# Performance work log

Measured on AMD Instinct MI355X. Metric: run time of the kernel, lower is better.

The kernel has to match this reference:

```python
import jax, jax.numpy as jnp
import numpy as np

DIM = 128
HEADS = 32
DIM_HEAD = 64
INNER = DIM * DIM_HEAD  # 8192, as written in the source (dim * dim_head)
D = INNER // HEADS      # 256 per-head dim
B, N = 1, 2048
ROT = 64                # partial rotary width (l)
SCALE = DIM ** (-0.5)   # source uses dim**-0.5, not head-dim


def _rotate_half(x):
    # x: [..., l]; split as (j d) with j=2 -> cat(-x2, x1)
    x1, x2 = jnp.split(x, 2, axis=-1)
    return jnp.concatenate((-x2, x1), axis=-1)


def _apply_rotary(q, k, freqs):
    # freqs: [n, l]; q,k: [b,h,n,d] with l <= d (partial rotary)
    l = freqs.shape[-1]
    cos, sin = jnp.cos(freqs), jnp.sin(freqs)  # broadcast over b,h
    ql, qr = q[..., :l], q[..., l:]
    kl, kr = k[..., :l], k[..., l:]
    ql = ql * cos + _rotate_half(ql) * sin
    kl = kl * cos + _rotate_half(kl) * sin
    return jnp.concatenate((ql, qr), axis=-1), jnp.concatenate((kl, kr), axis=-1)


def setup_inputs() -> dict:
    key = jax.random.key(0)
    k1, k2, k3, k4, k5 = jax.random.split(key, 5)
    return {
        "x": jax.random.normal(k1, (B, N, DIM), dtype=jnp.float32),
        "Wqkv": jax.random.normal(k2, (3 * INNER, DIM), dtype=jnp.float32) * 0.02,
        "Wproj": jax.random.normal(k3, (DIM, INNER), dtype=jnp.float32) * 0.02,
        "bproj": jax.random.normal(k4, (DIM,), dtype=jnp.float32) * 0.02,
        "rotary_pos_emb": jax.random.normal(k5, (N, ROT), dtype=jnp.float32),
    }


def reference(x, Wqkv, Wproj, bproj, rotary_pos_emb):
    b, n, _ = x.shape
    qkv = x @ Wqkv.T                                   # [b, n, 3*inner]
    qkv = qkv.reshape(b, n, 3, HEADS, D)               # (qkv h d) ordering
    qkv = jnp.transpose(qkv, (2, 0, 3, 1, 4))          # [3, b, h, n, d]
    q, k, v = qkv[0], qkv[1], qkv[2]
    q, k = _apply_rotary(q, k, rotary_pos_emb)
    energy = jnp.einsum("bhid,bhjd->bhij", q, k) * SCALE  # [b,h,n,n]
    attn = jax.nn.softmax(energy, axis=-1)
    out = jnp.einsum("bhij,bhjd->bhid", attn, v)       # [b,h,n,d]
    out = jnp.transpose(out, (0, 2, 1, 3)).reshape(b, n, INNER)
    return out @ Wproj.T + bproj
```

## Files before the change

### kernel.cpp

```cpp
#include <hip/hip_runtime.h>


typedef unsigned short u16;
typedef unsigned int u32;
typedef __attribute__((ext_vector_type(8))) u16 u16x8;
typedef __attribute__((ext_vector_type(8))) __bf16 bf16x8;
typedef __attribute__((ext_vector_type(4))) float f32x4;
typedef __attribute__((ext_vector_type(16))) float f32x16;
typedef __attribute__((ext_vector_type(4))) u32 u32x4;
typedef __attribute__((ext_vector_type(2))) u32 u32x2;

#define DEV static __device__ __forceinline__

DEV u16 f2b(float f) {
  __bf16 h = (__bf16)f;
  return __builtin_bit_cast(u16, h);
}
DEV float b2f(u16 b) {
  u32 u = ((u32)b) << 16;
  return __builtin_bit_cast(float, u);
}
DEV u32 pk2(float a, float b) { return (u32)f2b(a) | ((u32)f2b(b) << 16); }

DEV f32x4 mfma16(u16x8 a, u16x8 b, f32x4 c) {
  return __builtin_amdgcn_mfma_f32_16x16x32_bf16(
      __builtin_bit_cast(bf16x8, a), __builtin_bit_cast(bf16x8, b), c, 0, 0, 0);
}
DEV f32x16 mfma32(u16x8 a, u16x8 b, f32x16 c) {
  return __builtin_amdgcn_mfma_f32_32x32x16_bf16(
      __builtin_bit_cast(bf16x8, a), __builtin_bit_cast(bf16x8, b), c, 0, 0, 0);
}

DEV int swz(int row, int kelem, int rowBytes) {
  return row * rowBytes + ((kelem * 2) ^ ((row & 7) << 4));
}

DEV void dma16(const void* g, void* l) {
  __builtin_amdgcn_global_load_lds(
      (const __attribute__((address_space(1))) void*)g,
      (__attribute__((address_space(3))) void*)l, 16, 0, 0);
}

__global__ __launch_bounds__(256) void k_cvt(const float* __restrict__ src,
                                             u16* __restrict__ dst, int n8) {
  int i = blockIdx.x * 256 + threadIdx.x;
  if (i >= n8) return;
  const float4* s = (const float4*)src;
  float4 a = s[i * 2], b = s[i * 2 + 1];
  u16x8 o;
  o[0] = f2b(a.x); o[1] = f2b(a.y); o[2] = f2b(a.z); o[3] = f2b(a.w);
  o[4] = f2b(b.x); o[5] = f2b(b.y); o[6] = f2b(b.z); o[7] = f2b(b.w);
  *(u16x8*)(dst + (size_t)i * 8) = o;
}

__global__ __launch_bounds__(256) void k_qkv(const u16* __restrict__ xb,
                                             const u16* __restrict__ wb,
                                             u16* __restrict__ qw,
                                             u16* __restrict__ kw,
                                             u16* __restrict__ vw) {
  __shared__ char lds[65536];
  const int tid = threadIdx.x;
  const int rt = blockIdx.x % 192, nt = blockIdx.x / 192;
  const int r0 = rt * 128, n0 = nt * 128;
#pragma unroll
  for (int p = 0; p < 8; ++p) {
    int row = p * 16 + (tid >> 4);
    int k0 = (tid & 15) * 8;
    *(u16x8*)(lds + swz(row, k0, 256)) =
        *(const u16x8*)(wb + (size_t)(r0 + row) * 128 + k0);
    *(u16x8*)(lds + 32768 + swz(row, k0, 256)) =
        *(const u16x8*)(xb + (size_t)(n0 + row) * 128 + k0);
  }
  __syncthreads();
  const int wid = tid >> 6, lane = tid & 63, lq = lane & 15, g = lane >> 4;
  const int wr = wid >> 1, wn = wid & 1;
  const bool isV = (r0 >= 16384);
  f32x4 acc[4][4] = {};
#pragma unroll
  for (int ks = 0; ks < 4; ++ks) {
    u16x8 wa[4], xa[4];
#pragma unroll
    for (int i = 0; i < 4; ++i) {
      int rw = wr * 64 + i * 16 + lq;
      wa[i] = *(const u16x8*)(lds + swz(rw, ks * 32 + g * 8, 256));
      int rx = wn * 64 + i * 16 + lq;
      xa[i] = *(const u16x8*)(lds + 32768 + swz(rx, ks * 32 + g * 8, 256));
    }
    if (!isV) {
#pragma unroll
      for (int i = 0; i < 4; ++i)
#pragma unroll
        for (int j = 0; j < 4; ++j) acc[i][j] = mfma16(wa[i], xa[j], acc[i][j]);
    } else {
#pragma unroll
      for (int i = 0; i < 4; ++i)
#pragma unroll
        for (int j = 0; j < 4; ++j) acc[i][j] = mfma16(xa[j], wa[i], acc[i][j]);
    }
  }
  const float SMQ = 0.08838834764831845f * 1.4426950408889634f;
  if (!isV) {
#pragma unroll
    for (int i = 0; i < 4; ++i) {
      int rb = r0 + wr * 64 + i * 16 + g * 4;
      u16* dst0 = (rb >= 8192) ? kw : qw;
      float scl = (rb >= 8192) ? 1.0f : SMQ;
      int hd = rb & 8191;
      int h = hd >> 8, db = hd & 255;
#pragma unroll
      for (int j = 0; j < 4; ++j) {
        int n = n0 + wn * 64 + j * 16 + lq;
        u32x2 pk;
        pk.x = pk2(acc[i][j][0] * scl, acc[i][j][1] * scl);
        pk.y = pk2(acc[i][j][2] * scl, acc[i][j][3] * scl);
        *(u32x2*)(dst0 + ((size_t)h * 2048 + n) * 256 + db) = pk;
      }
    }
  } else {
#pragma unroll
    for (int i = 0; i < 4; ++i) {
      int rc = r0 - 16384 + wr * 64 + i * 16 + lq;
      int h = rc >> 8, d = rc & 255;
#pragma unroll
      for (int j = 0; j < 4; ++j) {
        int nb = n0 + wn * 64 + j * 16 + g * 4;
        u32x2 pk;
        pk.x = pk2(acc[i][j][0], acc[i][j][1]);
        pk.y = pk2(acc[i][j][2], acc[i][j][3]);
        *(u32x2*)(vw + ((size_t)h * 256 + d) * 2048 + nb) = pk;
      }
    }
  }
}

__global__ __launch_bounds__(256) void k_rope(u16* __restrict__ qw,
                                              u16* __restrict__ kw,
                                              const float* __restrict__ fr) {
  int idx = blockIdx.x * 256 + threadIdx.x;
  int seg = idx & 3;
  int n = (idx >> 2) & 2047;
  int h = (idx >> 13) & 31;
  u16* base = ((idx >> 18) ? kw : qw) + ((size_t)h * 2048 + n) * 256 + seg * 8;
  u16x8 lo = *(const u16x8*)base;
  u16x8 hi = *(const u16x8*)(base + 32);
  const float* f = fr + n * 64 + seg * 8;
  u16x8 nlo, nhi;
#pragma unroll
  for (int e = 0; e < 8; ++e) {
    float fl = f[e], fh = f[e + 32];
    float sl, cl, sh, ch;
    __sincosf(fl, &sl, &cl);
    __sincosf(fh, &sh, &ch);
    float a = b2f(lo[e]), b = b2f(hi[e]);
    nlo[e] = f2b(a * cl - b * sl);
    nhi[e] = f2b(b * ch + a * sh);
  }
  *(u16x8*)base = nlo;
  *(u16x8*)(base + 32) = nhi;
}

__global__ __launch_bounds__(512, 2) void k_attn(const u16* __restrict__ qw,
                                                 const u16* __restrict__ kw,
                                                 const u16* __restrict__ vw,
                                                 u16* __restrict__ ow) {
  __shared__ char lds[98304];
  const int tid = threadIdx.x;
  const int h = blockIdx.x & 31;
  const int qb = blockIdx.x >> 5;
  const int wid = tid >> 6, lane = tid & 63;
  const int l31 = lane & 31, h2 = lane >> 5;
  const int q0w = qb * 256 + wid * 32;
  const int lane16 = lane * 16;

  const u16* kbase = kw + (size_t)h * 2048 * 256;
  const u16* vbase = vw + (size_t)h * 256 * 2048;

  const bool isK = (wid < 4);
  const int dstslot = isK ? wid * 4 : 16 + (wid - 4) * 4;
  int off[4];
#pragma unroll
  for (int i = 0; i < 4; ++i) {
    if (isK) {
      int s = wid * 4 + i;
      off[i] = l31 * 256 + s * 16 + h2 * 8;
    } else {
      int u = (wid - 4) * 4 + i;
      off[i] = ((u >> 1) * 32 + l31) * 2048 + (u & 1) * 16 + h2 * 8;
    }
  }

  u16x8 qf[16];
  {
    const u16* qp = qw + ((size_t)h * 2048 + q0w + l31) * 256 + h2 * 8;
#pragma unroll
    for (int dt = 0; dt < 16; ++dt) qf[dt] = *(const u16x8*)(qp + dt * 16);
  }

  f32x16 oacc[8] = {};
  float mrun = -1e30f, lrun = 0.f;

#define STAGE(T, BUF)                                               \
  {                                                                 \
    const int kv0_ = (T) * 32;                                      \
    char* b_ = lds + (BUF) * 32768;                                 \
    if (isK) {                                                      \
      _Pragma("unroll") for (int i = 0; i < 4; ++i)                 \
          dma16(kbase + (size_t)kv0_ * 256 + off[i],                \
                b_ + (dstslot + i) * 1024);                         \
    } else {                                                        \
      _Pragma("unroll") for (int i = 0; i < 4; ++i)                 \
          dma16(vbase + kv0_ + off[i], b_ + (dstslot + i) * 1024);  \
    }                                                               \
  }

  STAGE(0, 0);
  STAGE(1, 1);
  int rb = 0, sb = 2;

  for (int t = 0; t < 64; ++t) {
    if (t < 63)
      asm volatile("s_waitcnt vmcnt(4)" ::: "memory");
    else
      asm volatile("s_waitcnt vmcnt(0)" ::: "memory");
    __builtin_amdgcn_s_barrier();
    asm volatile("" ::: "memory");
    if (t < 62) STAGE(t + 2, sb);

    const char* kb = lds + rb * 32768;

    f32x16 sa = {};
    __builtin_amdgcn_s_setprio(1);
#pragma unroll
    for (int dt = 0; dt < 16; ++dt) {
      u16x8 ka = *(const u16x8*)(kb + dt * 1024 + lane16);
      sa = mfma32(ka, qf[dt], sa);
    }
    __builtin_amdgcn_s_setprio(0);

    float m8[8];
#pragma unroll
    for (int r = 0; r < 8; ++r) m8[r] = fmaxf(sa[r], sa[r + 8]);
#pragma unroll
    for (int r = 0; r < 4; ++r) m8[r] = fmaxf(m8[r], m8[r + 4]);
    float mt = fmaxf(fmaxf(m8[0], m8[1]), fmaxf(m8[2], m8[3]));
    mt = fmaxf(mt, __shfl_xor(mt, 32));
    if (!__all(mt - mrun <= 8.0f)) {
      float mnew = fmaxf(mrun, mt);
      float corr = __builtin_amdgcn_exp2f(mrun - mnew);
      lrun *= corr;
#pragma unroll
      for (int dt = 0; dt < 8; ++dt)
#pragma unroll
        for (int r = 0; r < 16; ++r) oacc[dt][r] *= corr;
      mrun = mnew;
    }
    float p[16];
#pragma unroll
    for (int r = 0; r < 16; ++r)
      p[r] = __builtin_amdgcn_exp2f(sa[r] - mrun);
    float s8[8];
#pragma unroll
    for (int r = 0; r < 8; ++r) s8[r] = p[r] + p[r + 8];
#pragma unroll
    for (int r = 0; r < 4; ++r) s8[r] = s8[r] + s8[r + 4];
    float lt = (s8[0] + s8[1]) + (s8[2] + s8[3]);
    lt += __shfl_xor(lt, 32);
    lrun += lt;

    u32 pkk[8], xpk[8];
#pragma unroll
    for (int j = 0; j < 8; ++j) pkk[j] = pk2(p[2 * j], p[2 * j + 1]);
#pragma unroll
    for (int j = 0; j < 8; ++j) xpk[j] = (u32)__shfl_xor((int)pkk[j], 32);
    u32x4 b0v, b1v;
    b0v[0] = h2 ? xpk[2] : pkk[0];
    b0v[1] = h2 ? xpk[3] : pkk[1];
    b0v[2] = h2 ? pkk[2] : xpk[0];
    b0v[3] = h2 ? pkk[3] : xpk[1];
    b1v[0] = h2 ? xpk[6] : pkk[4];
    b1v[1] = h2 ? xpk[7] : pkk[5];
    b1v[2] = h2 ? pkk[6] : xpk[4];
    b1v[3] = h2 ? pkk[7] : xpk[5];
    u16x8 pb0 = __builtin_bit_cast(u16x8, b0v);
    u16x8 pb1 = __builtin_bit_cast(u16x8, b1v);

    __builtin_amdgcn_s_setprio(1);
#pragma unroll
    for (int dt = 0; dt < 8; ++dt) {
      u16x8 v0 = *(const u16x8*)(kb + 16384 + (dt * 2) * 1024 + lane16);
      oacc[dt] = mfma32(v0, pb0, oacc[dt]);
      u16x8 v1 = *(const u16x8*)(kb + 16384 + (dt * 2 + 1) * 1024 + lane16);
      oacc[dt] = mfma32(v1, pb1, oacc[dt]);
    }
    __builtin_amdgcn_s_setprio(0);

    rb = (rb == 2) ? 0 : rb + 1;
    sb = (sb == 2) ? 0 : sb + 1;
  }
#undef STAGE

  float inv = 1.0f / lrun;
  u16* orow = ow + (size_t)(q0w + l31) * 8192 + h * 256 + h2 * 4;
#pragma unroll
  for (int dt = 0; dt < 8; ++dt)
#pragma unroll
    for (int k = 0; k < 4; ++k) {
      u32x2 o2;
      o2.x = pk2(oacc[dt][4 * k] * inv, oacc[dt][4 * k + 1] * inv);
      o2.y = pk2(oacc[dt][4 * k + 2] * inv, oacc[dt][4 * k + 3] * inv);
      *(u32x2*)(orow + dt * 32 + k * 8) = o2;
    }
}

__global__ __launch_bounds__(256) void k_proj(const u16* __restrict__ ow,
                                              const u16* __restrict__ wp,
                                              float* __restrict__ part) {
  __shared__ char lds[49152];
  const int tid = threadIdx.x;
  const int nt = blockIdx.x >> 3, kc = blockIdx.x & 7;
  const int n0 = nt * 64, kb = kc * 1024;
  const int wid = tid >> 6, lane = tid & 63, lq = lane & 15, g = lane >> 4;
  f32x4 acc[8] = {};
  for (int kt = 0; kt < 8; ++kt) {
    int kk = kb + kt * 128;
#pragma unroll
    for (int p = 0; p < 4; ++p) {
      int nr = p * 16 + (tid >> 4);
      int k0 = (tid & 15) * 8;
      *(u16x8*)(lds + swz(nr, k0, 256)) =
          *(const u16x8*)(ow + (size_t)(n0 + nr) * 8192 + kk + k0);
    }
#pragma unroll
    for (int p = 0; p < 8; ++p) {
      int er = p * 16 + (tid >> 4);
      int k0 = (tid & 15) * 8;
      *(u16x8*)(lds + 16384 + swz(er, k0, 256)) =
          *(const u16x8*)(wp + (size_t)er * 8192 + kk + k0);
    }
    __syncthreads();
#pragma unroll
    for (int ks = 0; ks < 4; ++ks) {
      int nr = wid * 16 + lq;
      u16x8 oa = *(const u16x8*)(lds + swz(nr, ks * 32 + g * 8, 256));
#pragma unroll
      for (int ef = 0; ef < 8; ++ef) {
        int er = ef * 16 + lq;
        u16x8 wf = *(const u16x8*)(lds + 16384 + swz(er, ks * 32 + g * 8, 256));
        acc[ef] = mfma16(oa, wf, acc[ef]);
      }
    }
    __syncthreads();
  }
  float* pb = part + (size_t)kc * 262144;
#pragma unroll
  for (int ef = 0; ef < 8; ++ef)
#pragma unroll
    for (int r = 0; r < 4; ++r) {
      int n = n0 + wid * 16 + g * 4 + r;
      pb[n * 128 + ef * 16 + lq] = acc[ef][r];
    }
}

__global__ __launch_bounds__(256) void k_reduce(const float* __restrict__ part,
                                                const float* __restrict__ bias,
                                                float* __restrict__ out) {
  int i = blockIdx.x * 256 + threadIdx.x;
  float s = bias[i & 127];
#pragma unroll
  for (int c = 0; c < 8; ++c) s += part[(size_t)c * 262144 + i];
  out[i] = s;
}

extern "C" void kernel_launch(void* const* d_in, const int* in_sizes, int n_in,
                              void* d_out, int out_size, void* d_ws, size_t ws_size,
                              hipStream_t stream) {
  const float* x = (const float*)d_in[0];
  const float* wqkv = (const float*)d_in[1];
  const float* wproj = (const float*)d_in[2];
  const float* bproj = (const float*)d_in[3];
  const float* rope = (const float*)d_in[4];
  char* ws = (char*)d_ws;
  u16* xb    = (u16*)(ws);
  u16* wqkvb = (u16*)(ws + 524288);
  u16* wpb   = (u16*)(ws + 6815744);
  u16* qw    = (u16*)(ws + 8912896);
  u16* kw    = (u16*)(ws + 42467328);
  u16* vw    = (u16*)(ws + 76021760);
  u16* owv   = (u16*)(ws + 109576192);
  float* part = (float*)(ws + 8912896);

  k_cvt<<<128, 256, 0, stream>>>(x, xb, 32768);
  k_cvt<<<1536, 256, 0, stream>>>(wqkv, wqkvb, 393216);
  k_cvt<<<512, 256, 0, stream>>>(wproj, wpb, 131072);
  k_qkv<<<3072, 256, 0, stream>>>(xb, wqkvb, qw, kw, vw);
  k_rope<<<2048, 256, 0, stream>>>(qw, kw, rope);
  k_attn<<<256, 512, 0, stream>>>(qw, kw, vw, owv);
  k_proj<<<256, 256, 0, stream>>>(owv, wpb, part);
  k_reduce<<<1024, 256, 0, stream>>>(part, bproj, (float*)d_out);
}
```

Before: 229.4 us.

## Halve attention block size and switch to double-buffered K/V staging

The attention kernel now runs 256-thread blocks covering 128 queries each, launched as 512 blocks instead of 256 blocks of 512 threads. Every wave loads both K and V tiles rather than splitting the load roles, and the LDS ring shrinks from three buffers to two, with a full vmcnt(0) wait each iteration. The aim is more blocks to fill the GPU's compute units and lower LDS use per block. In exchange, prefetch depth drops to one stage and each K/V tile is loaded twice as many times across blocks.

```diff
diff --git a/kernel.cpp b/kernel.cpp
--- a/kernel.cpp
+++ b/kernel.cpp
@@ -159,34 +159,28 @@
   *(u16x8*)(base + 32) = nhi;
 }
 
-__global__ __launch_bounds__(512, 2) void k_attn(const u16* __restrict__ qw,
+__global__ __launch_bounds__(256, 2) void k_attn(const u16* __restrict__ qw,
                                                  const u16* __restrict__ kw,
                                                  const u16* __restrict__ vw,
                                                  u16* __restrict__ ow) {
-  __shared__ char lds[98304];
+  __shared__ char lds[65536];
   const int tid = threadIdx.x;
   const int h = blockIdx.x & 31;
   const int qb = blockIdx.x >> 5;
   const int wid = tid >> 6, lane = tid & 63;
   const int l31 = lane & 31, h2 = lane >> 5;
-  const int q0w = qb * 256 + wid * 32;
+  const int q0w = qb * 128 + wid * 32;
   const int lane16 = lane * 16;
 
   const u16* kbase = kw + (size_t)h * 2048 * 256;
   const u16* vbase = vw + (size_t)h * 256 * 2048;
 
-  const bool isK = (wid < 4);
-  const int dstslot = isK ? wid * 4 : 16 + (wid - 4) * 4;
-  int off[4];
+  int koff[4], voff[4];
 #pragma unroll
   for (int i = 0; i < 4; ++i) {
-    if (isK) {
-      int s = wid * 4 + i;
-      off[i] = l31 * 256 + s * 16 + h2 * 8;
-    } else {
-      int u = (wid - 4) * 4 + i;
-      off[i] = ((u >> 1) * 32 + l31) * 2048 + (u & 1) * 16 + h2 * 8;
-    }
+    int s = wid * 4 + i;
+    koff[i] = l31 * 256 + s * 16 + h2 * 8;
+    voff[i] = ((s >> 1) * 32 + l31) * 2048 + (s & 1) * 16 + h2 * 8;
   }
 
   u16x8 qf[16];
@@ -199,34 +193,27 @@
   f32x16 oacc[8] = {};
   float mrun = -1e30f, lrun = 0.f;
 
-#define STAGE(T, BUF)                                               \
-  {                                                                 \
-    const int kv0_ = (T) * 32;                                      \
-    char* b_ = lds + (BUF) * 32768;                                 \
-    if (isK) {                                                      \
-      _Pragma("unroll") for (int i = 0; i < 4; ++i)                 \
-          dma16(kbase + (size_t)kv0_ * 256 + off[i],                \
-                b_ + (dstslot + i) * 1024);                         \
-    } else {                                                        \
-      _Pragma("unroll") for (int i = 0; i < 4; ++i)                 \
-          dma16(vbase + kv0_ + off[i], b_ + (dstslot + i) * 1024);  \
-    }                                                               \
+#define STAGE(T, BUF)                                                 \
+  {                                                                   \
+    const int kv0_ = (T) * 32;                                        \
+    char* b_ = lds + (BUF) * 32768;                                   \
+    _Pragma("unroll") for (int i = 0; i < 4; ++i) {                   \
+      dma16(kbase + (size_t)kv0_ * 256 + koff[i],                     \
+            b_ + (wid * 4 + i) * 1024);                               \
+      dma16(vbase + kv0_ + voff[i],                                   \
+            b_ + 16384 + (wid * 4 + i) * 1024);                       \
+    }                                                                 \
   }
 
   STAGE(0, 0);
-  STAGE(1, 1);
-  int rb = 0, sb = 2;
 
   for (int t = 0; t < 64; ++t) {
-    if (t < 63)
-      asm volatile("s_waitcnt vmcnt(4)" ::: "memory");
-    else
-      asm volatile("s_waitcnt vmcnt(0)" ::: "memory");
+    asm volatile("s_waitcnt vmcnt(0)" ::: "memory");
     __builtin_amdgcn_s_barrier();
     asm volatile("" ::: "memory");
-    if (t < 62) STAGE(t + 2, sb);
-
-    const char* kb = lds + rb * 32768;
+    if (t < 63) STAGE(t + 1, (t + 1) & 1);
+
+    const char* kb = lds + (t & 1) * 32768;
 
     f32x16 sa = {};
     __builtin_amdgcn_s_setprio(1);
@@ -284,18 +271,16 @@
     u16x8 pb0 = __builtin_bit_cast(u16x8, b0v);
     u16x8 pb1 = __builtin_bit_cast(u16x8, b1v);
 
+    const char* vb = kb + 16384;
     __builtin_amdgcn_s_setprio(1);
 #pragma unroll
     for (int dt = 0; dt < 8; ++dt) {
-      u16x8 v0 = *(const u16x8*)(kb + 16384 + (dt * 2) * 1024 + lane16);
+      u16x8 v0 = *(const u16x8*)(vb + (dt * 2) * 1024 + lane16);
       oacc[dt] = mfma32(v0, pb0, oacc[dt]);
-      u16x8 v1 = *(const u16x8*)(kb + 16384 + (dt * 2 + 1) * 1024 + lane16);
+      u16x8 v1 = *(const u16x8*)(vb + (dt * 2 + 1) * 1024 + lane16);
       oacc[dt] = mfma32(v1, pb1, oacc[dt]);
     }
     __builtin_amdgcn_s_setprio(0);
-
-    rb = (rb == 2) ? 0 : rb + 1;
-    sb = (sb == 2) ? 0 : sb + 1;
   }
 #undef STAGE
 
@@ -394,7 +379,7 @@
   k_cvt<<<512, 256, 0, stream>>>(wproj, wpb, 131072);
   k_qkv<<<3072, 256, 0, stream>>>(xb, wqkvb, qw, kw, vw);
   k_rope<<<2048, 256, 0, stream>>>(qw, kw, rope);
-  k_attn<<<256, 512, 0, stream>>>(qw, kw, vw, owv);
+  k_attn<<<512, 256, 0, stream>>>(qw, kw, vw, owv);
   k_proj<<<256, 256, 0, stream>>>(owv, wpb, part);
   k_reduce<<<1024, 256, 0, stream>>>(part, bproj, (float*)d_out);
 }
```

Measured after the change: 242.3 us. 5.6% more time.
